# Optimization experiments

Hardware: AMD Instinct MI355X
Metric: run time of the kernel (lower is better)

## Reference

```python
import jax, jax.numpy as jnp
import numpy as np


def setup_inputs() -> dict:
    key = jax.random.key(0)
    k1, k2 = jax.random.split(key)
    B, N, D = 256, 50000, 2048
    queries = jax.random.normal(k1, (B, D), dtype=jnp.float32)
    bank = jax.random.normal(k2, (N, D), dtype=jnp.float32)
    return {"queries": queries, "bank": bank}


def reference(queries, bank):
    # Cosine similarity of every query against every bank row, fused as one
    # GEMM + row-norm scaling (original repeats the query N times per item
    # in a Python loop; math is identical).
    eps = jnp.float32(1e-12)
    q_norm = jnp.sqrt(jnp.sum(queries * queries, axis=1, keepdims=True))  # [B,1]
    b_norm = jnp.sqrt(jnp.sum(bank * bank, axis=1))                       # [N]
    dots = jnp.einsum('bd,nd->bn', queries, bank)                         # [B,N]
    scores = dots / jnp.maximum(q_norm * b_norm[None, :], eps)
    best_idx = jnp.argmax(scores, axis=1)  # retrieval result per batch item
    return best_idx, scores
```

## Files before the change

kernel.cpp:

```cpp
#include <hip/hip_runtime.h>
#include <stdint.h>

#define MQ 256
#define NB 50000
#define KD 2048
#define BN 64
#define BK 64
#define KT (KD / BK)
#define NBLK ((NB + BN - 1) / BN)

typedef __attribute__((ext_vector_type(8))) short bf16x8;
typedef __attribute__((ext_vector_type(4))) float f32x4;

__device__ __forceinline__ unsigned int pack_bf16(float a, float b) {
  unsigned int ua = __float_as_uint(a);
  ua += 0x7fffu + ((ua >> 16) & 1u);
  unsigned int ub = __float_as_uint(b);
  ub += 0x7fffu + ((ub >> 16) & 1u);
  return (ua >> 16) | (ub & 0xffff0000u);
}

__device__ __forceinline__ unsigned int ordf(float f) {
  unsigned int u = __float_as_uint(f);
  return (u & 0x80000000u) ? ~u : (u | 0x80000000u);
}
__device__ __forceinline__ float deordf(unsigned int e) {
  unsigned int u = (e & 0x80000000u) ? (e ^ 0x80000000u) : ~e;
  return __uint_as_float(u);
}

__device__ __forceinline__ float wave_sum(float v) {
#pragma unroll
  for (int o = 32; o > 0; o >>= 1) v += __shfl_down(v, o, 64);
  return v;
}

__global__ __launch_bounds__(256) void prep_q(const float* __restrict__ q,
                                              unsigned short* __restrict__ qbf,
                                              float* __restrict__ qn) {
  const int b = blockIdx.x, tid = threadIdx.x;
  const float* row = q + (size_t)b * KD;
  float4 v0 = *(const float4*)(row + tid * 8);
  float4 v1 = *(const float4*)(row + tid * 8 + 4);
  float sq = v0.x * v0.x + v0.y * v0.y + v0.z * v0.z + v0.w * v0.w +
             v1.x * v1.x + v1.y * v1.y + v1.z * v1.z + v1.w * v1.w;
  uint4 o;
  o.x = pack_bf16(v0.x, v0.y);
  o.y = pack_bf16(v0.z, v0.w);
  o.z = pack_bf16(v1.x, v1.y);
  o.w = pack_bf16(v1.z, v1.w);
  *(uint4*)(qbf + (size_t)b * KD + tid * 8) = o;
  sq = wave_sum(sq);
  __shared__ float s4[4];
  if ((tid & 63) == 0) s4[tid >> 6] = sq;
  __syncthreads();
  if (tid == 0) qn[b] = sqrtf(s4[0] + s4[1] + s4[2] + s4[3]);
}

__global__ __launch_bounds__(512, 4) void gemm_scores(
    const float* __restrict__ bank, const unsigned short* __restrict__ qbf,
    const float* __restrict__ qn, float* __restrict__ out_scores,
    unsigned long long* __restrict__ bm) {
  __shared__ alignas(16) unsigned short Bs[2][BN * BK];
  __shared__ float qn_s[MQ];
  __shared__ float bsq_s[512];
  __shared__ float bn_s[BN];

  const int tid = threadIdx.x;
  const int w = tid >> 6;
  const int lane = tid & 63;
  const int n0 = blockIdx.x * BN;

  if (tid < MQ) qn_s[tid] = qn[tid];

  f32x4 acc[2][4] = {};

  const int br = tid >> 3;
  const int bc = (tid & 7) * 8;
  const int be0 = bc ^ ((br & 7) * 8);
  int brow = n0 + br;
  if (brow >= NB) brow = NB - 1;
  const float* bsrc = bank + (size_t)brow * KD + bc;

  const int quad4 = lane >> 4;
  const unsigned short* ab0 =
      qbf + (size_t)(w * 32 + (lane & 15)) * KD + quad4 * 8;
  const unsigned short* ab1 = ab0 + (size_t)16 * KD;

  float bsq = 0.f;
  float4 g0, g1;

  g0 = *(const float4*)(bsrc);
  g1 = *(const float4*)(bsrc + 4);
  bsq += g0.x * g0.x + g0.y * g0.y + g0.z * g0.z + g0.w * g0.w +
         g1.x * g1.x + g1.y * g1.y + g1.z * g1.z + g1.w * g1.w;
  {
    uint4 pk;
    pk.x = pack_bf16(g0.x, g0.y);
    pk.y = pack_bf16(g0.z, g0.w);
    pk.z = pack_bf16(g1.x, g1.y);
    pk.w = pack_bf16(g1.z, g1.w);
    *(uint4*)&Bs[0][br * BK + be0] = pk;
  }
  bf16x8 aA0 = *(const bf16x8*)(ab0);
  bf16x8 aA1 = *(const bf16x8*)(ab0 + 32);
  bf16x8 aA2 = *(const bf16x8*)(ab1);
  bf16x8 aA3 = *(const bf16x8*)(ab1 + 32);
  g0 = *(const float4*)(bsrc + BK);
  g1 = *(const float4*)(bsrc + BK + 4);
  bf16x8 aB0, aB1, aB2, aB3;
  __syncthreads();

#define GBODY(KT_, C0, C1, C2, C3, N0_, N1_, N2_, N3_)                        \
  do {                                                                        \
    const int kt_ = (KT_);                                                    \
    if (kt_ + 1 < KT) {                                                       \
      N0_ = *(const bf16x8*)(ab0 + (kt_ + 1) * BK);                           \
      N1_ = *(const bf16x8*)(ab0 + (kt_ + 1) * BK + 32);                      \
      N2_ = *(const bf16x8*)(ab1 + (kt_ + 1) * BK);                           \
      N3_ = *(const bf16x8*)(ab1 + (kt_ + 1) * BK + 32);                      \
    }                                                                         \
    const unsigned short* bsp = Bs[kt_ & 1];                                  \
    _Pragma("unroll") for (int s = 0; s < 2; ++s) {                           \
      const int kx = (s * 32 + quad4 * 8) ^ ((lane & 7) * 8);                 \
      bf16x8 bfv[4];                                                          \
      _Pragma("unroll") for (int t = 0; t < 4; ++t) bfv[t] =                  \
          *(const bf16x8*)&bsp[(t * 16 + (lane & 15)) * BK + kx];             \
      _Pragma("unroll") for (int tn = 0; tn < 4; ++tn) {                      \
        acc[0][tn] = __builtin_amdgcn_mfma_f32_16x16x32_bf16(                 \
            s ? C1 : C0, bfv[tn], acc[0][tn], 0, 0, 0);                       \
        acc[1][tn] = __builtin_amdgcn_mfma_f32_16x16x32_bf16(                 \
            s ? C3 : C2, bfv[tn], acc[1][tn], 0, 0, 0);                       \
      }                                                                       \
    }                                                                         \
    if (kt_ + 1 < KT) {                                                       \
      bsq += g0.x * g0.x + g0.y * g0.y + g0.z * g0.z + g0.w * g0.w +          \
             g1.x * g1.x + g1.y * g1.y + g1.z * g1.z + g1.w * g1.w;           \
      uint4 pk;                                                               \
      pk.x = pack_bf16(g0.x, g0.y);                                           \
      pk.y = pack_bf16(g0.z, g0.w);                                           \
      pk.z = pack_bf16(g1.x, g1.y);                                           \
      pk.w = pack_bf16(g1.z, g1.w);                                           \
      *(uint4*)&Bs[(kt_ + 1) & 1][br * BK + be0] = pk;                        \
      if (kt_ + 2 < KT) {                                                     \
        const float* pp = bsrc + (kt_ + 2) * BK;                              \
        g0 = *(const float4*)(pp);                                            \
        g1 = *(const float4*)(pp + 4);                                        \
      }                                                                       \
      asm volatile("s_waitcnt lgkmcnt(0)\n\ts_barrier" ::: "memory");         \
    }                                                                         \
  } while (0)

  for (int kt = 0; kt < KT; kt += 2) {
    GBODY(kt, aA0, aA1, aA2, aA3, aB0, aB1, aB2, aB3);
    GBODY(kt + 1, aB0, aB1, aB2, aB3, aA0, aA1, aA2, aA3);
  }
#undef GBODY

  __syncthreads();
  bsq_s[tid] = bsq;
  __syncthreads();
  if (tid < BN) {
    float s = 0.f;
#pragma unroll
    for (int j = 0; j < 8; ++j) s += bsq_s[tid * 8 + j];
    bn_s[tid] = sqrtf(s);
  }
  __syncthreads();

  const int quad = lane >> 4, nl = lane & 15;
#pragma unroll
  for (int tm = 0; tm < 2; ++tm) {
#pragma unroll
    for (int r = 0; r < 4; ++r) {
      const int m = w * 32 + tm * 16 + quad * 4 + r;
      const float qm = qn_s[m];
      unsigned long long best = 0ull;
#pragma unroll
      for (int tn = 0; tn < 4; ++tn) {
        const int gn = n0 + tn * 16 + nl;
        if (gn < NB) {
          const float sc =
              acc[tm][tn][r] / fmaxf(qm * bn_s[tn * 16 + nl], 1e-12f);
          out_scores[(size_t)m * NB + gn] = sc;
          const unsigned long long pk =
              ((unsigned long long)ordf(sc) << 32) | (unsigned int)gn;
          best = pk > best ? pk : best;
        }
      }
#pragma unroll
      for (int mask = 1; mask < 16; mask <<= 1) {
        const unsigned long long o = __shfl_xor(best, mask, 64);
        best = o > best ? o : best;
      }
      if (nl == 0) bm[(size_t)m * NBLK + blockIdx.x] = best;
    }
  }
}

__global__ __launch_bounds__(256) void argmax_rescue(
    const unsigned long long* __restrict__ bm, const float* __restrict__ scores,
    const float* __restrict__ q, const float* __restrict__ bank,
    float* __restrict__ out_idx) {
  const int b = blockIdx.x, tid = threadIdx.x;
  const int w = tid >> 6, lane = tid & 63;
  const unsigned long long* rbm = bm + (size_t)b * NBLK;

  unsigned long long pmax = 0ull;
  for (int i = tid; i < NBLK; i += 256) {
    const unsigned long long v = rbm[i];
    pmax = v > pmax ? v : pmax;
  }
#pragma unroll
  for (int o = 32; o > 0; o >>= 1) {
    const unsigned long long v = __shfl_down(pmax, o, 64);
    pmax = v > pmax ? v : pmax;
  }
  __shared__ unsigned long long red[4];
  if (lane == 0) red[w] = pmax;
  __syncthreads();
  unsigned long long gmax = red[0];
#pragma unroll
  for (int i = 1; i < 4; ++i) gmax = red[i] > gmax ? red[i] : gmax;
  const float thr = deordf((unsigned int)(gmax >> 32)) - 2e-3f;

  __shared__ int cand[64];
  __shared__ int cnt;
  if (tid == 0) cnt = 0;
  __syncthreads();
  const float* srow = scores + (size_t)b * NB;
  for (int i = tid; i < NBLK; i += 256) {
    const float bmf = deordf((unsigned int)(rbm[i] >> 32));
    if (bmf >= thr) {
      const int base = i * BN;
      const int lim = min(BN, NB - base);
      for (int j = 0; j < lim; ++j) {
        if (srow[base + j] >= thr) {
          const int c = atomicAdd(&cnt, 1);
          if (c < 64) cand[c] = base + j;
        }
      }
    }
  }
  __syncthreads();
  const int nc = min(cnt, 64);

  __shared__ float dd[4], ss[4];
  float best = -1e30f;
  int bidx = 0x7fffffff;
  const float* qrow = q + (size_t)b * KD;
  for (int c = 0; c < nc; ++c) {
    const int idx = cand[c];
    const float* brow = bank + (size_t)idx * KD;
    float4 bv0 = *(const float4*)(brow + tid * 8);
    float4 bv1 = *(const float4*)(brow + tid * 8 + 4);
    float4 qv0 = *(const float4*)(qrow + tid * 8);
    float4 qv1 = *(const float4*)(qrow + tid * 8 + 4);
    float d = 0.f, s = 0.f;
    d = fmaf(qv0.x, bv0.x, d);
    s = fmaf(bv0.x, bv0.x, s);
    d = fmaf(qv0.y, bv0.y, d);
    s = fmaf(bv0.y, bv0.y, s);
    d = fmaf(qv0.z, bv0.z, d);
    s = fmaf(bv0.z, bv0.z, s);
    d = fmaf(qv0.w, bv0.w, d);
    s = fmaf(bv0.w, bv0.w, s);
    d = fmaf(qv1.x, bv1.x, d);
    s = fmaf(bv1.x, bv1.x, s);
    d = fmaf(qv1.y, bv1.y, d);
    s = fmaf(bv1.y, bv1.y, s);
    d = fmaf(qv1.z, bv1.z, d);
    s = fmaf(bv1.z, bv1.z, s);
    d = fmaf(qv1.w, bv1.w, d);
    s = fmaf(bv1.w, bv1.w, s);
    d = wave_sum(d);
    s = wave_sum(s);
    if (lane == 0) {
      dd[w] = d;
      ss[w] = s;
    }
    __syncthreads();
    const float dt = dd[0] + dd[1] + dd[2] + dd[3];
    const float st = ss[0] + ss[1] + ss[2] + ss[3];
    const float sc = dt / fmaxf(sqrtf(st), 1e-12f);
    if (sc > best || (sc == best && idx < bidx)) {
      best = sc;
      bidx = idx;
    }
    __syncthreads();
  }
  if (tid == 0) out_idx[b] = (float)bidx;
}

extern "C" void kernel_launch(void* const* d_in, const int* in_sizes, int n_in,
                              void* d_out, int out_size, void* d_ws,
                              size_t ws_size, hipStream_t stream) {
  const float* queries = (const float*)d_in[0];
  const float* bank = (const float*)d_in[1];
  float* out = (float*)d_out;
  float* out_scores = out + MQ;

  char* ws = (char*)d_ws;
  unsigned short* qbf = (unsigned short*)ws;
  float* qn = (float*)(ws + (size_t)MQ * KD * 2);
  unsigned long long* bm =
      (unsigned long long*)(ws + (size_t)MQ * KD * 2 + 2048);

  prep_q<<<MQ, 256, 0, stream>>>(queries, qbf, qn);
  gemm_scores<<<NBLK, 512, 0, stream>>>(bank, qbf, qn, out_scores, bm);
  argmax_rescue<<<MQ, 256, 0, stream>>>(bm, out_scores, queries, bank, out);
}
```

Baseline: 635.1 us.

## Quad-buffer bank tiles, prefetch two k-tiles ahead, halve barriers

```diff
diff --git a/kernel.cpp b/kernel.cpp
--- a/kernel.cpp
+++ b/kernel.cpp
@@ -57,11 +57,15 @@
   if (tid == 0) qn[b] = sqrtf(s4[0] + s4[1] + s4[2] + s4[3]);
 }
 
+#define BSQ8(G0, G1)                                                       \
+  (G0.x * G0.x + G0.y * G0.y + G0.z * G0.z + G0.w * G0.w + G1.x * G1.x +   \
+   G1.y * G1.y + G1.z * G1.z + G1.w * G1.w)
+
 __global__ __launch_bounds__(512, 4) void gemm_scores(
     const float* __restrict__ bank, const unsigned short* __restrict__ qbf,
     const float* __restrict__ qn, float* __restrict__ out_scores,
     unsigned long long* __restrict__ bm) {
-  __shared__ alignas(16) unsigned short Bs[2][BN * BK];
+  __shared__ alignas(16) unsigned short Bs[4][BN * BK];
   __shared__ float qn_s[MQ];
   __shared__ float bsq_s[512];
   __shared__ float bn_s[BN];
@@ -88,39 +92,51 @@
   const unsigned short* ab1 = ab0 + (size_t)16 * KD;
 
   float bsq = 0.f;
-  float4 g0, g1;
-
-  g0 = *(const float4*)(bsrc);
-  g1 = *(const float4*)(bsrc + 4);
-  bsq += g0.x * g0.x + g0.y * g0.y + g0.z * g0.z + g0.w * g0.w +
-         g1.x * g1.x + g1.y * g1.y + g1.z * g1.z + g1.w * g1.w;
+  float4 gA0, gA1, gB0, gB1;
+
+  gA0 = *(const float4*)(bsrc);
+  gA1 = *(const float4*)(bsrc + 4);
+  gB0 = *(const float4*)(bsrc + BK);
+  gB1 = *(const float4*)(bsrc + BK + 4);
+  bsq += BSQ8(gA0, gA1);
   {
     uint4 pk;
-    pk.x = pack_bf16(g0.x, g0.y);
-    pk.y = pack_bf16(g0.z, g0.w);
-    pk.z = pack_bf16(g1.x, g1.y);
-    pk.w = pack_bf16(g1.z, g1.w);
+    pk.x = pack_bf16(gA0.x, gA0.y);
+    pk.y = pack_bf16(gA0.z, gA0.w);
+    pk.z = pack_bf16(gA1.x, gA1.y);
+    pk.w = pack_bf16(gA1.z, gA1.w);
     *(uint4*)&Bs[0][br * BK + be0] = pk;
+  }
+  bsq += BSQ8(gB0, gB1);
+  {
+    uint4 pk;
+    pk.x = pack_bf16(gB0.x, gB0.y);
+    pk.y = pack_bf16(gB0.z, gB0.w);
+    pk.z = pack_bf16(gB1.x, gB1.y);
+    pk.w = pack_bf16(gB1.z, gB1.w);
+    *(uint4*)&Bs[1][br * BK + be0] = pk;
   }
   bf16x8 aA0 = *(const bf16x8*)(ab0);
   bf16x8 aA1 = *(const bf16x8*)(ab0 + 32);
   bf16x8 aA2 = *(const bf16x8*)(ab1);
   bf16x8 aA3 = *(const bf16x8*)(ab1 + 32);
-  g0 = *(const float4*)(bsrc + BK);
-  g1 = *(const float4*)(bsrc + BK + 4);
   bf16x8 aB0, aB1, aB2, aB3;
   __syncthreads();
-
-#define GBODY(KT_, C0, C1, C2, C3, N0_, N1_, N2_, N3_)                        \
+  gA0 = *(const float4*)(bsrc + 2 * BK);
+  gA1 = *(const float4*)(bsrc + 2 * BK + 4);
+  gB0 = *(const float4*)(bsrc + 3 * BK);
+  gB1 = *(const float4*)(bsrc + 3 * BK + 4);
+
+#define HALF(KT_, CA0, CA1, CA2, CA3, NA0, NA1, NA2, NA3, G0, G1)             \
   do {                                                                        \
     const int kt_ = (KT_);                                                    \
     if (kt_ + 1 < KT) {                                                       \
-      N0_ = *(const bf16x8*)(ab0 + (kt_ + 1) * BK);                           \
-      N1_ = *(const bf16x8*)(ab0 + (kt_ + 1) * BK + 32);                      \
-      N2_ = *(const bf16x8*)(ab1 + (kt_ + 1) * BK);                           \
-      N3_ = *(const bf16x8*)(ab1 + (kt_ + 1) * BK + 32);                      \
+      NA0 = *(const bf16x8*)(ab0 + (kt_ + 1) * BK);                           \
+      NA1 = *(const bf16x8*)(ab0 + (kt_ + 1) * BK + 32);                      \
+      NA2 = *(const bf16x8*)(ab1 + (kt_ + 1) * BK);                           \
+      NA3 = *(const bf16x8*)(ab1 + (kt_ + 1) * BK + 32);                      \
     }                                                                         \
-    const unsigned short* bsp = Bs[kt_ & 1];                                  \
+    const unsigned short* bsp = Bs[kt_ & 3];                                  \
     _Pragma("unroll") for (int s = 0; s < 2; ++s) {                           \
       const int kx = (s * 32 + quad4 * 8) ^ ((lane & 7) * 8);                 \
       bf16x8 bfv[4];                                                          \
@@ -128,34 +144,34 @@
           *(const bf16x8*)&bsp[(t * 16 + (lane & 15)) * BK + kx];             \
       _Pragma("unroll") for (int tn = 0; tn < 4; ++tn) {                      \
         acc[0][tn] = __builtin_amdgcn_mfma_f32_16x16x32_bf16(                 \
-            s ? C1 : C0, bfv[tn], acc[0][tn], 0, 0, 0);                       \
+            s ? CA1 : CA0, bfv[tn], acc[0][tn], 0, 0, 0);                     \
         acc[1][tn] = __builtin_amdgcn_mfma_f32_16x16x32_bf16(                 \
-            s ? C3 : C2, bfv[tn], acc[1][tn], 0, 0, 0);                       \
+            s ? CA3 : CA2, bfv[tn], acc[1][tn], 0, 0, 0);                     \
       }                                                                       \
     }                                                                         \
-    if (kt_ + 1 < KT) {                                                       \
-      bsq += g0.x * g0.x + g0.y * g0.y + g0.z * g0.z + g0.w * g0.w +          \
-             g1.x * g1.x + g1.y * g1.y + g1.z * g1.z + g1.w * g1.w;           \
+    if (kt_ + 2 < KT) {                                                       \
+      bsq += BSQ8(G0, G1);                                                    \
       uint4 pk;                                                               \
-      pk.x = pack_bf16(g0.x, g0.y);                                           \
-      pk.y = pack_bf16(g0.z, g0.w);                                           \
-      pk.z = pack_bf16(g1.x, g1.y);                                           \
-      pk.w = pack_bf16(g1.z, g1.w);                                           \
-      *(uint4*)&Bs[(kt_ + 1) & 1][br * BK + be0] = pk;                        \
-      if (kt_ + 2 < KT) {                                                     \
-        const float* pp = bsrc + (kt_ + 2) * BK;                              \
-        g0 = *(const float4*)(pp);                                            \
-        g1 = *(const float4*)(pp + 4);                                        \
+      pk.x = pack_bf16(G0.x, G0.y);                                           \
+      pk.y = pack_bf16(G0.z, G0.w);                                           \
+      pk.z = pack_bf16(G1.x, G1.y);                                           \
+      pk.w = pack_bf16(G1.z, G1.w);                                           \
+      *(uint4*)&Bs[(kt_ + 2) & 3][br * BK + be0] = pk;                        \
+      if (kt_ + 4 < KT) {                                                     \
+        const float* pp = bsrc + (kt_ + 4) * BK;                              \
+        G0 = *(const float4*)(pp);                                            \
+        G1 = *(const float4*)(pp + 4);                                        \
       }                                                                       \
-      asm volatile("s_waitcnt lgkmcnt(0)\n\ts_barrier" ::: "memory");         \
     }                                                                         \
   } while (0)
 
   for (int kt = 0; kt < KT; kt += 2) {
-    GBODY(kt, aA0, aA1, aA2, aA3, aB0, aB1, aB2, aB3);
-    GBODY(kt + 1, aB0, aB1, aB2, aB3, aA0, aA1, aA2, aA3);
-  }
-#undef GBODY
+    HALF(kt, aA0, aA1, aA2, aA3, aB0, aB1, aB2, aB3, gA0, gA1);
+    HALF(kt + 1, aB0, aB1, aB2, aB3, aA0, aA1, aA2, aA3, gB0, gB1);
+    if (kt + 2 < KT)
+      asm volatile("s_waitcnt lgkmcnt(0)\n\ts_barrier" ::: "memory");
+  }
+#undef HALF
 
   __syncthreads();
   bsq_s[tid] = bsq;
```

Result: no change. 641.2 us (+1.0%).

## Stage query tiles in LDS via direct global-to-LDS loads with triple-buffered pipeline

Applied to the files above, without the earlier changes.

```diff
diff --git a/kernel.cpp b/kernel.cpp
--- a/kernel.cpp
+++ b/kernel.cpp
@@ -11,6 +11,12 @@
 
 typedef __attribute__((ext_vector_type(8))) short bf16x8;
 typedef __attribute__((ext_vector_type(4))) float f32x4;
+
+#define SFENCE()                       \
+  do {                                 \
+    asm volatile("" ::: "memory");     \
+    __builtin_amdgcn_sched_barrier(0); \
+  } while (0)
 
 __device__ __forceinline__ unsigned int pack_bf16(float a, float b) {
   unsigned int ua = __float_as_uint(a);
@@ -57,11 +63,16 @@
   if (tid == 0) qn[b] = sqrtf(s4[0] + s4[1] + s4[2] + s4[3]);
 }
 
-__global__ __launch_bounds__(512, 4) void gemm_scores(
+#define BSQ8(G0, G1)                                                     \
+  (G0.x * G0.x + G0.y * G0.y + G0.z * G0.z + G0.w * G0.w + G1.x * G1.x + \
+   G1.y * G1.y + G1.z * G1.z + G1.w * G1.w)
+
+__global__ __launch_bounds__(512, 2) void gemm_scores(
     const float* __restrict__ bank, const unsigned short* __restrict__ qbf,
     const float* __restrict__ qn, float* __restrict__ out_scores,
     unsigned long long* __restrict__ bm) {
-  __shared__ alignas(16) unsigned short Bs[2][BN * BK];
+  __shared__ alignas(16) unsigned short As[3][MQ * BK];
+  __shared__ alignas(16) unsigned short Bs[3][BN * BK];
   __shared__ float qn_s[MQ];
   __shared__ float bsq_s[512];
   __shared__ float bn_s[BN];
@@ -82,80 +93,122 @@
   if (brow >= NB) brow = NB - 1;
   const float* bsrc = bank + (size_t)brow * KD + bc;
 
+  const int agr = tid >> 3;
+  const int acs = ((lane & 7) ^ (lane >> 3)) * 8;
+  const unsigned short* asrc0 = qbf + (size_t)agr * KD + acs;
+  const int adst = agr * BK + (lane & 7) * 8;
+
   const int quad4 = lane >> 4;
-  const unsigned short* ab0 =
-      qbf + (size_t)(w * 32 + (lane & 15)) * KD + quad4 * 8;
-  const unsigned short* ab1 = ab0 + (size_t)16 * KD;
+  const int l15 = lane & 15;
+  const int arow0 = (w * 32 + l15) * BK;
+  const int arow1 = (w * 32 + 16 + l15) * BK;
+  const int kxbase = (lane & 7) * 8;
 
   float bsq = 0.f;
-  float4 g0, g1;
-
-  g0 = *(const float4*)(bsrc);
-  g1 = *(const float4*)(bsrc + 4);
-  bsq += g0.x * g0.x + g0.y * g0.y + g0.z * g0.z + g0.w * g0.w +
-         g1.x * g1.x + g1.y * g1.y + g1.z * g1.z + g1.w * g1.w;
-  {
-    uint4 pk;
-    pk.x = pack_bf16(g0.x, g0.y);
-    pk.y = pack_bf16(g0.z, g0.w);
-    pk.z = pack_bf16(g1.x, g1.y);
-    pk.w = pack_bf16(g1.z, g1.w);
-    *(uint4*)&Bs[0][br * BK + be0] = pk;
-  }
-  bf16x8 aA0 = *(const bf16x8*)(ab0);
-  bf16x8 aA1 = *(const bf16x8*)(ab0 + 32);
-  bf16x8 aA2 = *(const bf16x8*)(ab1);
-  bf16x8 aA3 = *(const bf16x8*)(ab1 + 32);
-  g0 = *(const float4*)(bsrc + BK);
-  g1 = *(const float4*)(bsrc + BK + 4);
-  bf16x8 aB0, aB1, aB2, aB3;
-  __syncthreads();
-
-#define GBODY(KT_, C0, C1, C2, C3, N0_, N1_, N2_, N3_)                        \
-  do {                                                                        \
-    const int kt_ = (KT_);                                                    \
-    if (kt_ + 1 < KT) {                                                       \
-      N0_ = *(const bf16x8*)(ab0 + (kt_ + 1) * BK);                           \
-      N1_ = *(const bf16x8*)(ab0 + (kt_ + 1) * BK + 32);                      \
-      N2_ = *(const bf16x8*)(ab1 + (kt_ + 1) * BK);                           \
-      N3_ = *(const bf16x8*)(ab1 + (kt_ + 1) * BK + 32);                      \
-    }                                                                         \
-    const unsigned short* bsp = Bs[kt_ & 1];                                  \
-    _Pragma("unroll") for (int s = 0; s < 2; ++s) {                           \
-      const int kx = (s * 32 + quad4 * 8) ^ ((lane & 7) * 8);                 \
-      bf16x8 bfv[4];                                                          \
-      _Pragma("unroll") for (int t = 0; t < 4; ++t) bfv[t] =                  \
-          *(const bf16x8*)&bsp[(t * 16 + (lane & 15)) * BK + kx];             \
-      _Pragma("unroll") for (int tn = 0; tn < 4; ++tn) {                      \
-        acc[0][tn] = __builtin_amdgcn_mfma_f32_16x16x32_bf16(                 \
-            s ? C1 : C0, bfv[tn], acc[0][tn], 0, 0, 0);                       \
-        acc[1][tn] = __builtin_amdgcn_mfma_f32_16x16x32_bf16(                 \
-            s ? C3 : C2, bfv[tn], acc[1][tn], 0, 0, 0);                       \
-      }                                                                       \
-    }                                                                         \
-    if (kt_ + 1 < KT) {                                                       \
-      bsq += g0.x * g0.x + g0.y * g0.y + g0.z * g0.z + g0.w * g0.w +          \
-             g1.x * g1.x + g1.y * g1.y + g1.z * g1.z + g1.w * g1.w;           \
-      uint4 pk;                                                               \
-      pk.x = pack_bf16(g0.x, g0.y);                                           \
-      pk.y = pack_bf16(g0.z, g0.w);                                           \
-      pk.z = pack_bf16(g1.x, g1.y);                                           \
-      pk.w = pack_bf16(g1.z, g1.w);                                           \
-      *(uint4*)&Bs[(kt_ + 1) & 1][br * BK + be0] = pk;                        \
-      if (kt_ + 2 < KT) {                                                     \
-        const float* pp = bsrc + (kt_ + 2) * BK;                              \
-        g0 = *(const float4*)(pp);                                            \
-        g1 = *(const float4*)(pp + 4);                                        \
-      }                                                                       \
-      asm volatile("s_waitcnt lgkmcnt(0)\n\ts_barrier" ::: "memory");         \
-    }                                                                         \
+  float4 gP0, gP1, gQ0, gQ1;
+
+#define ISSUE_A(T_)                                                          \
+  {                                                                          \
+    unsigned short* dslot = &As[(T_) % 3][0];                                \
+    const unsigned short* s0 = asrc0 + (size_t)(T_)*BK;                      \
+    _Pragma("unroll") for (int i = 0; i < 4; ++i) {                          \
+      __builtin_amdgcn_global_load_lds(                                      \
+          (const __attribute__((address_space(1)))                           \
+               unsigned int*)(s0 + (size_t)i * 64 * KD),                     \
+          (__attribute__((address_space(3)))                                 \
+               unsigned int*)(dslot + i * 64 * BK + adst),                   \
+          16, 0, 0);                                                         \
+    }                                                                        \
+  }
+
+#define LOAD_B(T_, G0_, G1_)                  \
+  {                                           \
+    const float* pp = bsrc + (size_t)(T_)*BK; \
+    G0_ = *(const float4*)(pp);               \
+    G1_ = *(const float4*)(pp + 4);           \
+  }
+
+#define PACK_B(T_, G0_, G1_)                    \
+  {                                             \
+    bsq += BSQ8(G0_, G1_);                      \
+    uint4 pk;                                   \
+    pk.x = pack_bf16(G0_.x, G0_.y);             \
+    pk.y = pack_bf16(G0_.z, G0_.w);             \
+    pk.z = pack_bf16(G1_.x, G1_.y);             \
+    pk.w = pack_bf16(G1_.z, G1_.w);             \
+    *(uint4*)&Bs[(T_) % 3][br * BK + be0] = pk; \
+  }
+
+#define COMPUTE(T_)                                                          \
+  {                                                                          \
+    const unsigned short* Asl = &As[(T_) % 3][0];                            \
+    const unsigned short* Bsl = &Bs[(T_) % 3][0];                            \
+    _Pragma("unroll") for (int s = 0; s < 2; ++s) {                          \
+      const int kx = (s * 32 + quad4 * 8) ^ kxbase;                          \
+      bf16x8 af0 = *(const bf16x8*)&Asl[arow0 + kx];                         \
+      bf16x8 af1 = *(const bf16x8*)&Asl[arow1 + kx];                         \
+      bf16x8 bfv[4];                                                         \
+      _Pragma("unroll") for (int t = 0; t < 4; ++t) bfv[t] =                 \
+          *(const bf16x8*)&Bsl[(t * 16 + l15) * BK + kx];                    \
+      _Pragma("unroll") for (int tn = 0; tn < 4; ++tn) {                     \
+        acc[0][tn] = __builtin_amdgcn_mfma_f32_16x16x32_bf16(                \
+            af0, bfv[tn], acc[0][tn], 0, 0, 0);                              \
+        acc[1][tn] = __builtin_amdgcn_mfma_f32_16x16x32_bf16(                \
+            af1, bfv[tn], acc[1][tn], 0, 0, 0);                              \
+      }                                                                      \
+    }                                                                        \
+  }
+
+#define WAITBAR(VM_)                                                   \
+  asm volatile("s_waitcnt vmcnt(" #VM_ ") lgkmcnt(0)" ::: "memory");   \
+  __builtin_amdgcn_s_barrier();                                        \
+  __builtin_amdgcn_sched_barrier(0);
+
+#define BODY(T_, G0_, G1_, DOA_, DOB_, VM_)             \
+  do {                                                  \
+    if (DOA_) {                                         \
+      ISSUE_A((T_) + 2);                                \
+    }                                                   \
+    SFENCE();                                           \
+    COMPUTE(T_);                                        \
+    SFENCE();                                           \
+    PACK_B((T_) + 1, G0_, G1_);                         \
+    SFENCE();                                           \
+    if (DOB_) {                                         \
+      LOAD_B((T_) + 3, G0_, G1_);                       \
+      SFENCE();                                         \
+    }                                                   \
+    WAITBAR(VM_)                                        \
   } while (0)
 
-  for (int kt = 0; kt < KT; kt += 2) {
-    GBODY(kt, aA0, aA1, aA2, aA3, aB0, aB1, aB2, aB3);
-    GBODY(kt + 1, aB0, aB1, aB2, aB3, aA0, aA1, aA2, aA3);
-  }
-#undef GBODY
+  LOAD_B(0, gP0, gP1);
+  PACK_B(0, gP0, gP1);
+  SFENCE();
+  ISSUE_A(0);
+  SFENCE();
+  LOAD_B(1, gQ0, gQ1);
+  SFENCE();
+  ISSUE_A(1);
+  SFENCE();
+  LOAD_B(2, gP0, gP1);
+  SFENCE();
+  WAITBAR(8)
+
+  for (int t = 0; t < KT - 4; t += 2) {
+    BODY(t, gQ0, gQ1, 1, 1, 8);
+    BODY(t + 1, gP0, gP1, 1, 1, 8);
+  }
+  BODY(KT - 4, gQ0, gQ1, 1, 1, 8);
+  BODY(KT - 3, gP0, gP1, 1, 0, 6);
+  BODY(KT - 2, gQ0, gQ1, 0, 0, 0);
+  COMPUTE(KT - 1);
+
+#undef BODY
+#undef WAITBAR
+#undef COMPUTE
+#undef PACK_B
+#undef LOAD_B
+#undef ISSUE_A
 
   __syncthreads();
   bsq_s[tid] = bsq;
```

Result: slower. 662.7 us (+4.3%).
